# Kernel optimization log

Measured on AMD Instinct MI355X. Metric: run time of the kernel, lower is better.

The kernel has to match this reference:

```python
import jax, jax.numpy as jnp
import numpy as np

SCALE = 1.0  # noise std used in the Gaussian log-pdf
HIGH = jax.lax.Precision.HIGHEST


def setup_inputs() -> dict:
    key = jax.random.key(0)
    k1, k2, k3 = jax.random.split(key, 3)
    B, N, D, T = 64, 256, 64, 4096
    data = jax.random.normal(k1, (B, N, D), dtype=jnp.float32)
    targets = jax.random.normal(k2, (B, N), dtype=jnp.float32)
    task_pool = jax.random.normal(k3, (T, D, 1), dtype=jnp.float32)
    return {"data": data, "targets": targets, "task_pool": task_pool}


def reference(data, targets, task_pool):
    # data: [B, N, D], targets: [B, N], task_pool: [T, D, 1]
    W = jnp.squeeze(task_pool).T  # [D, T]
    # Per-point, per-task Gaussian log-likelihood of targets under each task weight.
    Z = jnp.einsum('bnd,dt->bnt', data, W, precision=HIGH)  # [B, N, T]
    resid = targets[:, :, None] - Z
    logp = jax.scipy.stats.norm.logpdf(resid, loc=0.0, scale=SCALE)  # [B, N, T]
    # alpha for step i (i >= 1) is the cumulative log-lik over points 0..i-1.
    cum = jnp.cumsum(logp, axis=1)          # [B, N, T]
    alphas = cum[:, :-1]                    # [B, N-1, T], alphas[:, i-1] = alpha at step i
    post = jax.nn.softmax(alphas, axis=-1)  # posterior over tasks per step
    # MMSE weight per step: posterior-weighted average of task weights.
    w_mmse = jnp.einsum('bit,dt->bid', post, W, precision=HIGH)  # [B, N-1, D]
    preds_rest = jnp.einsum('bid,bid->bi', data[:, 1:], w_mmse)  # [B, N-1]
    # Step 0: prior mean weight (uniform average over task pool).
    pred0 = data[:, 0] @ W.mean(axis=1)  # [B]
    return jnp.concatenate([pred0[:, None], preds_rest], axis=1)  # [B, N]
```

## Files before the change

kernel.cpp:

```cpp
#include <hip/hip_runtime.h>
#include <math.h>

#define BB 64
#define NN 256
#define DD 64
#define TT 4096

#define NCH 16
#define CT (TT/NCH)
#define THREADS 512
#define WAVES 8
#define NB 16
#define NGRP (NN/NB)
#define BN (BB*NN)

#define TILE_BYTES 4096
#define TILES_BYTES ((size_t)BB*NGRP*TILE_BYTES)

#define NHL2E (-0.72134752044448170368f)

typedef __bf16 bf16x8 __attribute__((ext_vector_type(8)));
typedef float  f32x4  __attribute__((ext_vector_type(4)));

#define SHR1 0x111
#define SHR2 0x112
#define SHR4 0x114
#define SHR8 0x118

template<int C>
__device__ __forceinline__ float dppf(float x) {
  return __int_as_float(__builtin_amdgcn_update_dpp(
      0, __float_as_int(x), C, 0xf, 0xf, true));
}

__device__ __forceinline__ float bcast15(float x) {
  return __int_as_float(__builtin_amdgcn_ds_swizzle(__float_as_int(x), 0x1F0));
}

__device__ __forceinline__ unsigned short f2bf(float f) {
  unsigned int u = __float_as_uint(f);
  unsigned int r = u + 0x7FFFu + ((u >> 16) & 1u);
  return (unsigned short)(r >> 16);
}
__device__ __forceinline__ float bf2f(unsigned short h) {
  return __uint_as_float(((unsigned int)h) << 16);
}

#define GLOAD_LDS16(gp, lp_) \
  __builtin_amdgcn_global_load_lds((const __attribute__((address_space(1))) void*)(gp), \
                                   (__attribute__((address_space(3))) void*)(lp_), 16, 0, 0)

union FragU { unsigned int u[4]; bf16x8 v; };

__global__ __launch_bounds__(256)
void mmse_phase0(const float* __restrict__ data, unsigned char* __restrict__ tiles)
{
  const int e  = blockIdx.x * 256 + threadIdx.x;
  const int k2 = e & 31;
  const int n  = (e >> 5) & 255;
  const int b  = e >> 13;
  const float2 q = ((const float2*)data)[e];
  const unsigned short h0 = f2bf(q.x), h1 = f2bf(q.y);
  const unsigned short g0 = f2bf(q.x - bf2f(h0)), g1 = f2bf(q.y - bf2f(h1));
  const int nr = n & 15;
  const int logical = nr * 128 + k2 * 4;
  const int phys = logical ^ ((nr & 7) << 4);
  unsigned char* tp = tiles + (size_t)(b * NGRP + (n >> 4)) * TILE_BYTES;
  *(unsigned int*)(tp + phys)        = (unsigned int)h0 | ((unsigned int)h1 << 16);
  *(unsigned int*)(tp + 2048 + phys) = (unsigned int)g0 | ((unsigned int)g1 << 16);
}

__device__ __forceinline__ void merge8(const float2 (*sb)[16], int lane,
                                       float* __restrict__ part, size_t obase) {
  const int col = lane & 15;
  float2 p0 = sb[0][col];
  float M = p0.x, S = 1.f, V = p0.y;
  #pragma unroll
  for (int w = 1; w < WAVES; ++w) {
    float2 pw = sb[w][col];
    float mn = fmaxf(M, pw.x);
    float ea = __builtin_amdgcn_exp2f(M - mn);
    float eb = __builtin_amdgcn_exp2f(pw.x - mn);
    S = S * ea + eb;
    V = fmaf(V, ea, pw.y * eb);
    M = mn;
  }
  if (lane < 16) {
    const size_t o = (obase + (size_t)col * NCH) * 2;
    part[o]     = M + __log2f(S);
    part[o + 1] = V / S;
  }
}

__global__ __launch_bounds__(THREADS, 4)
void mmse_phase1(const unsigned char* __restrict__ tiles,
                 const float* __restrict__ targets,
                 const float* __restrict__ Wp,
                 float* __restrict__ part)
{
  const int bx   = blockIdx.x;
  const int b    = bx >> 4;
  const int ch   = bx & 15;
  const int tid  = threadIdx.x;
  const int lane = tid & 63;
  const int wave = tid >> 6;

  __shared__ uint4  dbufq[2][256];
  __shared__ float  tgl[NN];
  __shared__ float2 sbuf[2][WAVES][16];

  unsigned char* dbufc = (unsigned char*)dbufq;

  bf16x8 aH[2][2], aL[2][2];
  {
    const int tb = ch * CT + wave * 32;
    #pragma unroll
    for (int tile = 0; tile < 2; ++tile) {
      #pragma unroll
      for (int s = 0; s < 2; ++s) {
        const int row = tb + tile * 16 + (lane & 15);
        const int kb  = s * 32 + (lane >> 4) * 8;
        const float* wp = Wp + (size_t)row * DD + kb;
        FragU hu, lu;
        #pragma unroll
        for (int jj = 0; jj < 4; ++jj) {
          const float f0 = wp[2 * jj], f1 = wp[2 * jj + 1];
          const unsigned short h0 = f2bf(f0), h1 = f2bf(f1);
          const unsigned short g0 = f2bf(f0 - bf2f(h0)), g1 = f2bf(f1 - bf2f(h1));
          hu.u[jj] = (unsigned int)h0 | ((unsigned int)h1 << 16);
          lu.u[jj] = (unsigned int)g0 | ((unsigned int)g1 << 16);
        }
        aH[tile][s] = hu.v; aL[tile][s] = lu.v;
      }
    }
  }

  if (wave == 0)
    GLOAD_LDS16(targets + (size_t)b * NN + lane * 4, tgl);
  if (wave < 4)
    GLOAD_LDS16(tiles + (size_t)(b * NGRP) * TILE_BYTES + wave * 1024 + lane * 16,
                dbufc + wave * 1024);
  __syncthreads();

  float c8[8];
  #pragma unroll
  for (int i = 0; i < 8; ++i) c8[i] = 0.f;

  const size_t obase0 = (size_t)(b * NN) * NCH + ch;

  #pragma unroll 1
  for (int g = 0; g < NGRP; ++g) {
    const int buf = g & 1;
    const unsigned char* bp = dbufc + buf * 4096;
    const int ra = ((lane & 15) * 128 + (lane >> 4) * 16) ^ ((lane & 7) << 4);
    bf16x8 bh0 = *(const bf16x8*)(bp + ra);
    bf16x8 bh1 = *(const bf16x8*)(bp + (ra ^ 64));
    bf16x8 bl0 = *(const bf16x8*)(bp + 2048 + ra);
    bf16x8 bl1 = *(const bf16x8*)(bp + 2048 + (ra ^ 64));

    if (g + 1 < NGRP && wave < 4)
      GLOAD_LDS16(tiles + (size_t)(b * NGRP + g + 1) * TILE_BYTES + wave * 1024 + lane * 16,
                  dbufc + (buf ^ 1) * 4096 + wave * 1024);

    if (g > 0 && wave == ((g - 1) & 7))
      merge8(sbuf[(g - 1) & 1], lane, part, obase0 + (size_t)((g - 1) * NB) * NCH);

    f32x4 zz[2];
    zz[0] = (f32x4)(0.f); zz[1] = (f32x4)(0.f);
    zz[0] = __builtin_amdgcn_mfma_f32_16x16x32_bf16(aH[0][0], bh0, zz[0], 0, 0, 0);
    zz[0] = __builtin_amdgcn_mfma_f32_16x16x32_bf16(aH[0][0], bl0, zz[0], 0, 0, 0);
    zz[0] = __builtin_amdgcn_mfma_f32_16x16x32_bf16(aL[0][0], bh0, zz[0], 0, 0, 0);
    zz[0] = __builtin_amdgcn_mfma_f32_16x16x32_bf16(aH[0][1], bh1, zz[0], 0, 0, 0);
    zz[0] = __builtin_amdgcn_mfma_f32_16x16x32_bf16(aH[0][1], bl1, zz[0], 0, 0, 0);
    zz[0] = __builtin_amdgcn_mfma_f32_16x16x32_bf16(aL[0][1], bh1, zz[0], 0, 0, 0);
    zz[1] = __builtin_amdgcn_mfma_f32_16x16x32_bf16(aH[1][0], bh0, zz[1], 0, 0, 0);
    zz[1] = __builtin_amdgcn_mfma_f32_16x16x32_bf16(aH[1][0], bl0, zz[1], 0, 0, 0);
    zz[1] = __builtin_amdgcn_mfma_f32_16x16x32_bf16(aL[1][0], bh0, zz[1], 0, 0, 0);
    zz[1] = __builtin_amdgcn_mfma_f32_16x16x32_bf16(aH[1][1], bh1, zz[1], 0, 0, 0);
    zz[1] = __builtin_amdgcn_mfma_f32_16x16x32_bf16(aH[1][1], bl1, zz[1], 0, 0, 0);
    zz[1] = __builtin_amdgcn_mfma_f32_16x16x32_bf16(aL[1][1], bh1, zz[1], 0, 0, 0);

    const float tgf = tgl[g * 16 + (lane & 15)];

    float alpha[8];
    float mloc = -3.4e38f;
    #pragma unroll
    for (int tile = 0; tile < 2; ++tile) {
      #pragma unroll
      for (int r = 0; r < 4; ++r) {
        const int t8 = tile * 4 + r;
        const float z  = zz[tile][r];
        const float rr = tgf - z;
        const float lp = rr * rr * NHL2E;
        float x = lp;
        x += dppf<SHR1>(x);
        x += dppf<SHR2>(x);
        x += dppf<SHR4>(x);
        x += dppf<SHR8>(x);
        const float tot = bcast15(x);
        const float a_ = c8[t8] + (x - lp);
        alpha[t8] = a_;
        c8[t8] += tot;
        mloc = fmaxf(mloc, a_);
      }
    }
    float m = fmaxf(mloc, __shfl_xor(mloc, 16));
    m = fmaxf(m, __shfl_xor(m, 32));
    float sv = 0.f, vv = 0.f;
    #pragma unroll
    for (int tile = 0; tile < 2; ++tile) {
      #pragma unroll
      for (int r = 0; r < 4; ++r) {
        const float p = __builtin_amdgcn_exp2f(alpha[tile * 4 + r] - m);
        sv += p;
        vv = fmaf(p, zz[tile][r], vv);
      }
    }
    sv += __shfl_xor(sv, 16); sv += __shfl_xor(sv, 32);
    vv += __shfl_xor(vv, 16); vv += __shfl_xor(vv, 32);
    if (lane < 16) {
      float2 lr;
      lr.x = m + __log2f(sv);
      lr.y = vv / sv;
      sbuf[buf][wave][lane] = lr;
    }

    __syncthreads();
  }

  if (wave == ((NGRP - 1) & 7))
    merge8(sbuf[(NGRP - 1) & 1], lane, part, obase0 + (size_t)((NGRP - 1) * NB) * NCH);
}

__global__ __launch_bounds__(256)
void mmse_phase2(const float* __restrict__ part, float* __restrict__ out)
{
  const int gid  = blockIdx.x * 256 + threadIdx.x;
  const int idx  = gid >> 1;
  const int half = gid & 1;
  const float2* __restrict__ p = (const float2*)part + (size_t)idx * NCH + half * 8;
  float M = -3.4e38f, S = 0.f, V = 0.f;
  #pragma unroll
  for (int c = 0; c < 8; ++c) {
    const float2 q = p[c];
    const float mn = fmaxf(M, q.x);
    const float ea = __builtin_amdgcn_exp2f(M - mn);
    const float eb = __builtin_amdgcn_exp2f(q.x - mn);
    S = fmaf(S, ea, eb);
    V = fmaf(V, ea, q.y * eb);
    M = mn;
  }
  const float m2 = __shfl_xor(M, 1), s2 = __shfl_xor(S, 1), v2 = __shfl_xor(V, 1);
  const float mn = fmaxf(M, m2);
  const float ea = __builtin_amdgcn_exp2f(M - mn);
  const float eb = __builtin_amdgcn_exp2f(m2 - mn);
  S = fmaf(S, ea, s2 * eb);
  V = fmaf(V, ea, v2 * eb);
  if (half == 0) out[idx] = V / S;
}

extern "C" void kernel_launch(void* const* d_in, const int* in_sizes, int n_in,
                              void* d_out, int out_size, void* d_ws, size_t ws_size,
                              hipStream_t stream)
{
  const float* data      = (const float*)d_in[0];
  const float* targets   = (const float*)d_in[1];
  const float* task_pool = (const float*)d_in[2];
  float* out = (float*)d_out;

  unsigned char* tiles = (unsigned char*)d_ws;
  float* part = (float*)((unsigned char*)d_ws + TILES_BYTES);

  hipLaunchKernelGGL(mmse_phase0, dim3(BB * NN * DD / 2 / 256), dim3(256), 0, stream,
                     data, tiles);
  hipLaunchKernelGGL(mmse_phase1, dim3(BB * NCH), dim3(THREADS), 0, stream,
                     tiles, targets, task_pool, part);
  hipLaunchKernelGGL(mmse_phase2, dim3(2 * BN / 256), dim3(256), 0, stream,
                     part, out);
}
```

Before: 122.2 us.

## Fuse bf16 hi/lo split of data into phase1 with register-staged prefetch

Removes the separate phase0 kernel that converted data into swizzled bf16 hi/lo tiles in global workspace. Phase1 now loads fp32 data directly, keeps the next group in registers while the current one computes, and writes the split into the alternate LDS buffer before the barrier. This saves a kernel launch and a write-then-reread of the workspace tiles. The cost is that each of the 16 chunk blocks per batch redoes the conversion, and the VGPRs and ALU work in the main loop go up.

```diff
diff --git a/kernel.cpp b/kernel.cpp
--- a/kernel.cpp
+++ b/kernel.cpp
@@ -14,9 +14,6 @@
 #define NGRP (NN/NB)
 #define BN (BB*NN)
 
-#define TILE_BYTES 4096
-#define TILES_BYTES ((size_t)BB*NGRP*TILE_BYTES)
-
 #define NHL2E (-0.72134752044448170368f)
 
 typedef __bf16 bf16x8 __attribute__((ext_vector_type(8)));
@@ -52,26 +49,8 @@
 
 union FragU { unsigned int u[4]; bf16x8 v; };
 
-__global__ __launch_bounds__(256)
-void mmse_phase0(const float* __restrict__ data, unsigned char* __restrict__ tiles)
-{
-  const int e  = blockIdx.x * 256 + threadIdx.x;
-  const int k2 = e & 31;
-  const int n  = (e >> 5) & 255;
-  const int b  = e >> 13;
-  const float2 q = ((const float2*)data)[e];
-  const unsigned short h0 = f2bf(q.x), h1 = f2bf(q.y);
-  const unsigned short g0 = f2bf(q.x - bf2f(h0)), g1 = f2bf(q.y - bf2f(h1));
-  const int nr = n & 15;
-  const int logical = nr * 128 + k2 * 4;
-  const int phys = logical ^ ((nr & 7) << 4);
-  unsigned char* tp = tiles + (size_t)(b * NGRP + (n >> 4)) * TILE_BYTES;
-  *(unsigned int*)(tp + phys)        = (unsigned int)h0 | ((unsigned int)h1 << 16);
-  *(unsigned int*)(tp + 2048 + phys) = (unsigned int)g0 | ((unsigned int)g1 << 16);
-}
-
 __device__ __forceinline__ void merge8(const float2 (*sb)[16], int lane,
-                                       float* __restrict__ part, size_t obase) {
+                                       float2* __restrict__ part, size_t obase) {
   const int col = lane & 15;
   float2 p0 = sb[0][col];
   float M = p0.x, S = 1.f, V = p0.y;
@@ -86,17 +65,18 @@
     M = mn;
   }
   if (lane < 16) {
-    const size_t o = (obase + (size_t)col * NCH) * 2;
-    part[o]     = M + __log2f(S);
-    part[o + 1] = V / S;
+    float2 lr;
+    lr.x = M + __log2f(S);
+    lr.y = V / S;
+    part[obase + (size_t)col * NCH] = lr;
   }
 }
 
 __global__ __launch_bounds__(THREADS, 4)
-void mmse_phase1(const unsigned char* __restrict__ tiles,
+void mmse_phase1(const float* __restrict__ data,
                  const float* __restrict__ targets,
                  const float* __restrict__ Wp,
-                 float* __restrict__ part)
+                 float2* __restrict__ part)
 {
   const int bx   = blockIdx.x;
   const int b    = bx >> 4;
@@ -137,9 +117,19 @@
 
   if (wave == 0)
     GLOAD_LDS16(targets + (size_t)b * NN + lane * 4, tgl);
-  if (wave < 4)
-    GLOAD_LDS16(tiles + (size_t)(b * NGRP) * TILE_BYTES + wave * 1024 + lane * 16,
-                dbufc + wave * 1024);
+
+  const float* __restrict__ dbase = data + (size_t)b * NN * DD;
+  const int sn  = tid >> 5;
+  const int sk2 = tid & 31;
+  const int sphys = (sn * 128 + sk2 * 4) ^ ((sn & 7) << 4);
+
+  {
+    const float2 q = *(const float2*)(dbase + (size_t)sn * DD + sk2 * 2);
+    const unsigned short h0 = f2bf(q.x), h1 = f2bf(q.y);
+    const unsigned short g0 = f2bf(q.x - bf2f(h0)), g1 = f2bf(q.y - bf2f(h1));
+    *(unsigned int*)(dbufc + sphys)        = (unsigned int)h0 | ((unsigned int)h1 << 16);
+    *(unsigned int*)(dbufc + 2048 + sphys) = (unsigned int)g0 | ((unsigned int)g1 << 16);
+  }
   __syncthreads();
 
   float c8[8];
@@ -158,9 +148,9 @@
     bf16x8 bl0 = *(const bf16x8*)(bp + 2048 + ra);
     bf16x8 bl1 = *(const bf16x8*)(bp + 2048 + (ra ^ 64));
 
-    if (g + 1 < NGRP && wave < 4)
-      GLOAD_LDS16(tiles + (size_t)(b * NGRP + g + 1) * TILE_BYTES + wave * 1024 + lane * 16,
-                  dbufc + (buf ^ 1) * 4096 + wave * 1024);
+    float2 q;
+    if (g + 1 < NGRP)
+      q = *(const float2*)(dbase + (size_t)((g + 1) * NB + sn) * DD + sk2 * 2);
 
     if (g > 0 && wave == ((g - 1) & 7))
       merge8(sbuf[(g - 1) & 1], lane, part, obase0 + (size_t)((g - 1) * NB) * NCH);
@@ -225,6 +215,13 @@
       sbuf[buf][wave][lane] = lr;
     }
 
+    if (g + 1 < NGRP) {
+      const unsigned short h0 = f2bf(q.x), h1 = f2bf(q.y);
+      const unsigned short g0 = f2bf(q.x - bf2f(h0)), g1 = f2bf(q.y - bf2f(h1));
+      unsigned char* wb = dbufc + (buf ^ 1) * 4096;
+      *(unsigned int*)(wb + sphys)        = (unsigned int)h0 | ((unsigned int)h1 << 16);
+      *(unsigned int*)(wb + 2048 + sphys) = (unsigned int)g0 | ((unsigned int)g1 << 16);
+    }
     __syncthreads();
   }
 
@@ -268,13 +265,10 @@
   const float* task_pool = (const float*)d_in[2];
   float* out = (float*)d_out;
 
-  unsigned char* tiles = (unsigned char*)d_ws;
-  float* part = (float*)((unsigned char*)d_ws + TILES_BYTES);
-
-  hipLaunchKernelGGL(mmse_phase0, dim3(BB * NN * DD / 2 / 256), dim3(256), 0, stream,
-                     data, tiles);
+  float2* part = (float2*)d_ws;
+
   hipLaunchKernelGGL(mmse_phase1, dim3(BB * NCH), dim3(THREADS), 0, stream,
-                     tiles, targets, task_pool, part);
+                     data, targets, task_pool, part);
   hipLaunchKernelGGL(mmse_phase2, dim3(2 * BN / 256), dim3(256), 0, stream,
-                     part, out);
-}
+                     (const float*)part, out);
+}
```

Measured after the change: 120.3 us. No clear change (-1.5%).
